# Kernel optimization log

Measured on AMD Instinct MI355X. Metric: run time of the kernel, lower is better.

## Reference

```python
import jax, jax.numpy as jnp
import numpy as np

D_ENC = 512
D_DEC = 512
D_JOINT = D_ENC + D_DEC  # 1024
V = 1024


def setup_inputs() -> dict:
    key = jax.random.key(0)
    ks = jax.random.split(key, 8)
    s = lambda fan_in: 1.0 / np.sqrt(fan_in)
    return {
        "encoder_output": jax.random.normal(ks[0], (8, 200, D_ENC), dtype=jnp.float32),
        "decoder_output": jax.random.normal(ks[1], (8, 50, D_DEC), dtype=jnp.float32),
        "W_enc": jax.random.uniform(ks[2], (D_JOINT, D_ENC), jnp.float32, -s(D_ENC), s(D_ENC)),
        "b_enc": jax.random.uniform(ks[3], (D_JOINT,), jnp.float32, -s(D_ENC), s(D_ENC)),
        "W_dec": jax.random.uniform(ks[4], (D_JOINT, D_DEC), jnp.float32, -s(D_DEC), s(D_DEC)),
        "b_dec": jax.random.uniform(ks[5], (D_JOINT,), jnp.float32, -s(D_DEC), s(D_DEC)),
        "W_fc": jax.random.uniform(ks[6], (V, D_JOINT), jnp.float32, -s(D_JOINT), s(D_JOINT)),
        "b_fc": jax.random.uniform(ks[7], (V,), jnp.float32, -s(D_JOINT), s(D_JOINT)),
    }


def reference(encoder_output, decoder_output, W_enc, b_enc, W_dec, b_dec, W_fc, b_fc):
    # enc: (B, T, D_JOINT); dec: (B, U, D_JOINT)
    enc = jnp.einsum('btd,jd->btj', encoder_output, W_enc) + b_enc
    dec = jnp.einsum('bud,jd->buj', decoder_output, W_dec) + b_dec
    # broadcast join: (B, T, U, D_JOINT)
    combined = enc[:, :, None, :] + dec[:, None, :, :]
    logits = jnp.einsum('btuj,vj->btuv', jnp.tanh(combined), W_fc) + b_fc
    return jax.nn.log_softmax(logits, axis=-1)
```

## Files before the change

### kernel.cpp

```cpp
#include <hip/hip_runtime.h>
#include <hip/hip_bf16.h>
#include <hip/hip_fp8.h>

#define TT 200
#define UU 50
#define BB 8
#define DJ 1024
#define DE 512
#define VV 1024
#define M_TOTAL (BB*TT*UU)
#define MB 80
#define NITER 32
#define WINV (1.0f/32.0f)

typedef float f32x4 __attribute__((ext_vector_type(4)));

__device__ __forceinline__ float fast_tanh(float x) {
    float e = __expf(2.f * x);
    return 1.f - 2.f / (e + 1.f);
}

__device__ __forceinline__ unsigned char f2fp8(float x) {
    return __hip_fp8_e4m3(x).__x;
}

__device__ __forceinline__ unsigned long long tanh_pack_fp8(float4 e0, float4 e1, float4 d0, float4 d1) {
    unsigned long long r;
    r  = (unsigned long long)f2fp8(fast_tanh(e0.x + d0.x));
    r |= (unsigned long long)f2fp8(fast_tanh(e0.y + d0.y)) << 8;
    r |= (unsigned long long)f2fp8(fast_tanh(e0.z + d0.z)) << 16;
    r |= (unsigned long long)f2fp8(fast_tanh(e0.w + d0.w)) << 24;
    r |= (unsigned long long)f2fp8(fast_tanh(e1.x + d1.x)) << 32;
    r |= (unsigned long long)f2fp8(fast_tanh(e1.y + d1.y)) << 40;
    r |= (unsigned long long)f2fp8(fast_tanh(e1.z + d1.z)) << 48;
    r |= (unsigned long long)f2fp8(fast_tanh(e1.w + d1.w)) << 56;
    return r;
}

__global__ void k_wfct(const float* __restrict__ w, unsigned char* __restrict__ o) {
    const int G = blockIdx.x * 256 + threadIdx.x;
    const int gk = G >> 10, n = G & 1023;
    const float* src = w + (size_t)n * DJ + gk * 8;
    float4 a = *(const float4*)(src);
    float4 b = *(const float4*)(src + 4);
    unsigned long long r;
    r  = (unsigned long long)f2fp8(a.x * 32.f);
    r |= (unsigned long long)f2fp8(a.y * 32.f) << 8;
    r |= (unsigned long long)f2fp8(a.z * 32.f) << 16;
    r |= (unsigned long long)f2fp8(a.w * 32.f) << 24;
    r |= (unsigned long long)f2fp8(b.x * 32.f) << 32;
    r |= (unsigned long long)f2fp8(b.y * 32.f) << 40;
    r |= (unsigned long long)f2fp8(b.z * 32.f) << 48;
    r |= (unsigned long long)f2fp8(b.w * 32.f) << 56;
    *(unsigned long long*)(o + (size_t)G * 8) = r;
}

__global__ __launch_bounds__(256) void k_proj2(const float* __restrict__ enc,
                                               const float* __restrict__ dec,
                                               const float* __restrict__ W_enc,
                                               const float* __restrict__ b_enc,
                                               const float* __restrict__ W_dec,
                                               const float* __restrict__ b_dec,
                                               float* __restrict__ encp,
                                               float* __restrict__ decp) {
    __shared__ float in_s[16][DE];
    const bool isDec = blockIdx.x >= 100;
    const float* in  = isDec ? dec   : enc;
    const float* W   = isDec ? W_dec : W_enc;
    const float* bia = isDec ? b_dec : b_enc;
    float* out       = isDec ? decp  : encp;
    const int NR     = isDec ? (BB*UU) : (BB*TT);
    const int m0 = (isDec ? (blockIdx.x - 100) : blockIdx.x) * 16;
    const int tid = threadIdx.x;
    #pragma unroll
    for (int it = 0; it < 8; ++it) {
        int idx = tid + it * 256;
        int r = idx >> 7, c = (idx & 127) << 2;
        *(float4*)&in_s[r][c] = *(const float4*)(in + (size_t)(m0 + r) * DE + c);
    }
    __syncthreads();
    const int j = blockIdx.y * 256 + tid;
    const float4* wr = (const float4*)(W + (size_t)j * DE);
    float acc[16];
    #pragma unroll
    for (int r = 0; r < 16; ++r) acc[r] = 0.f;
    for (int d4 = 0; d4 < DE / 4; ++d4) {
        float4 w = wr[d4];
        #pragma unroll
        for (int r = 0; r < 16; ++r) {
            float4 x = *(const float4*)&in_s[r][d4 << 2];
            acc[r] += x.x * w.x + x.y * w.y + x.z * w.z + x.w * w.w;
        }
    }
    float bv = bia[j];
    const int gk = j >> 3, kl = j & 7;
    #pragma unroll
    for (int r = 0; r < 16; ++r)
        out[((size_t)gk * NR + (m0 + r)) * 8 + kl] = acc[r] + bv;
}

__global__ __launch_bounds__(512, 2) void k_joint(const float* __restrict__ encp,
                                                  const float* __restrict__ decp,
                                                  const unsigned char* __restrict__ wfc8,
                                                  const float* __restrict__ bfc,
                                                  float* __restrict__ out) {
    __shared__ unsigned char As[81920];
    __shared__ float red[8][MB];

    const int tid = threadIdx.x;
    const int wave = tid >> 6, lane = tid & 63;
    const int g = lane >> 4, ln = lane & 15;
    const int bid = blockIdx.x;
    const int m0 = bid * MB;

    for (int r = 0; r < 20; ++r) {
        const int gidx = r * 512 + tid;
        const int gkf = gidx / MB;
        const int m = gidx - gkf * MB;
        const int mrow = m0 + m;
        const int b = mrow / (TT * UU);
        const int rem = mrow - b * (TT * UU);
        const int t = rem / UU;
        const int u = rem - t * UU;
        const float* ep = encp + ((size_t)gkf * (BB * TT) + b * TT + t) * 8;
        const float* dp = decp + ((size_t)gkf * (BB * UU) + b * UU + u) * 8;
        float4 e0 = *(const float4*)(ep);
        float4 e1 = *(const float4*)(ep + 4);
        float4 d0 = *(const float4*)(dp);
        float4 d1 = *(const float4*)(dp + 4);
        *(unsigned long long*)&As[(size_t)gidx * 8] = tanh_pack_fp8(e0, e1, d0, d1);
    }

    f32x4 acc[5][8];
    #pragma unroll
    for (int mf = 0; mf < 5; ++mf)
        #pragma unroll
        for (int nf = 0; nf < 8; ++nf)
            acc[mf][nf] = (f32x4){0.f, 0.f, 0.f, 0.f};

    __syncthreads();

    const unsigned char* bbase = wfc8 + (size_t)(wave * 128 + ln) * 8;

    for (int t = 0; t < NITER; ++t) {
        const int kb = (t + bid) & 31;
        long afr[5];
        #pragma unroll
        for (int mf = 0; mf < 5; ++mf)
            afr[mf] = *(const long*)&As[(size_t)((kb * 4 + g) * MB + mf * 16 + ln) * 8];
        const unsigned char* bchunk = bbase + (size_t)(kb * 4 + g) * 1024 * 8;
        #pragma unroll
        for (int nf = 0; nf < 8; ++nf) {
            long bfr = *(const long*)(bchunk + (size_t)nf * 16 * 8);
            #pragma unroll
            for (int mf = 0; mf < 5; ++mf)
                acc[mf][nf] = __builtin_amdgcn_mfma_f32_16x16x32_fp8_fp8(afr[mf], bfr, acc[mf][nf], 0, 0, 0);
        }
    }

    float bv[8];
    #pragma unroll
    for (int nf = 0; nf < 8; ++nf) bv[nf] = bfc[wave * 128 + nf * 16 + ln];
    #pragma unroll
    for (int mf = 0; mf < 5; ++mf)
        #pragma unroll
        for (int nf = 0; nf < 8; ++nf)
            #pragma unroll
            for (int j = 0; j < 4; ++j)
                acc[mf][nf][j] = acc[mf][nf][j] * WINV + bv[nf];

    float rmx[5][4];
    #pragma unroll
    for (int mf = 0; mf < 5; ++mf)
        #pragma unroll
        for (int j = 0; j < 4; ++j) {
            float mx = -3.0e38f;
            #pragma unroll
            for (int nf = 0; nf < 8; ++nf) mx = fmaxf(mx, acc[mf][nf][j]);
            #pragma unroll
            for (int s = 1; s < 16; s <<= 1) mx = fmaxf(mx, __shfl_xor(mx, s));
            rmx[mf][j] = mx;
        }
    if (ln == 0) {
        #pragma unroll
        for (int mf = 0; mf < 5; ++mf)
            #pragma unroll
            for (int j = 0; j < 4; ++j)
                red[wave][mf * 16 + g * 4 + j] = rmx[mf][j];
    }
    __syncthreads();
    #pragma unroll
    for (int mf = 0; mf < 5; ++mf)
        #pragma unroll
        for (int j = 0; j < 4; ++j) {
            const int r = mf * 16 + g * 4 + j;
            float mx = red[0][r];
            #pragma unroll
            for (int w = 1; w < 8; ++w) mx = fmaxf(mx, red[w][r]);
            rmx[mf][j] = mx;
        }
    __syncthreads();

    float rsm[5][4];
    #pragma unroll
    for (int mf = 0; mf < 5; ++mf)
        #pragma unroll
        for (int j = 0; j < 4; ++j) {
            float s = 0.f;
            #pragma unroll
            for (int nf = 0; nf < 8; ++nf) s += __expf(acc[mf][nf][j] - rmx[mf][j]);
            #pragma unroll
            for (int t2 = 1; t2 < 16; t2 <<= 1) s += __shfl_xor(s, t2);
            rsm[mf][j] = s;
        }
    if (ln == 0) {
        #pragma unroll
        for (int mf = 0; mf < 5; ++mf)
            #pragma unroll
            for (int j = 0; j < 4; ++j)
                red[wave][mf * 16 + g * 4 + j] = rsm[mf][j];
    }
    __syncthreads();
    #pragma unroll
    for (int mf = 0; mf < 5; ++mf)
        #pragma unroll
        for (int j = 0; j < 4; ++j) {
            const int r = mf * 16 + g * 4 + j;
            float s = 0.f;
            #pragma unroll
            for (int w = 0; w < 8; ++w) s += red[w][r];
            const float lse = rmx[mf][j] + __logf(s);
            float* op = out + (size_t)(m0 + r) * VV + wave * 128 + ln;
            #pragma unroll
            for (int nf = 0; nf < 8; ++nf)
                __builtin_nontemporal_store(acc[mf][nf][j] - lse, op + nf * 16);
        }
}

extern "C" void kernel_launch(void* const* d_in, const int* in_sizes, int n_in,
                              void* d_out, int out_size, void* d_ws, size_t ws_size,
                              hipStream_t stream) {
    const float* enc   = (const float*)d_in[0];
    const float* dec   = (const float*)d_in[1];
    const float* W_enc = (const float*)d_in[2];
    const float* b_enc = (const float*)d_in[3];
    const float* W_dec = (const float*)d_in[4];
    const float* b_dec = (const float*)d_in[5];
    const float* W_fc  = (const float*)d_in[6];
    const float* b_fc  = (const float*)d_in[7];
    float* out = (float*)d_out;

    float* encp = (float*)d_ws;
    float* decp = encp + (size_t)BB * TT * DJ;
    unsigned char* wfc8 = (unsigned char*)(decp + (size_t)BB * UU * DJ);

    k_wfct<<<(VV * DJ) / (256 * 8), 256, 0, stream>>>(W_fc, wfc8);
    k_proj2<<<dim3(125, DJ / 256), 256, 0, stream>>>(enc, dec, W_enc, b_enc, W_dec, b_dec, encp, decp);
    k_joint<<<M_TOTAL / MB, 512, 0, stream>>>(encp, decp, wfc8, b_fc, out);
}
```

Before: 325.7 us.

## Relayout FP8 operands for 16-byte loads and double-buffer K-loop fragments

Rearranges the FP8 W_fc buffer and the shared-memory A tile so each lane reads two consecutive K-steps as one 16-byte vector. This halves the number of load instructions per MFMA. The K loop now runs 16 iterations, each with two MFMA substeps, and software-pipelines them by prefetching the next iteration's A and B fragments into alternate register sets while the current MFMAs execute. This is meant to hide global and LDS load latency behind compute. The cost is higher register pressure at 512 threads with 2 blocks per SM, which could cause spills.

Result: slower. 405.9 us (+24.6%).

```diff
diff --git a/kernel.cpp b/kernel.cpp
--- a/kernel.cpp
+++ b/kernel.cpp
@@ -10,10 +10,10 @@
 #define VV 1024
 #define M_TOTAL (BB*TT*UU)
 #define MB 80
-#define NITER 32
 #define WINV (1.0f/32.0f)
 
 typedef float f32x4 __attribute__((ext_vector_type(4)));
+typedef long long2_t __attribute__((ext_vector_type(2)));
 
 __device__ __forceinline__ float fast_tanh(float x) {
     float e = __expf(2.f * x);
@@ -52,7 +52,8 @@
     r |= (unsigned long long)f2fp8(b.y * 32.f) << 40;
     r |= (unsigned long long)f2fp8(b.z * 32.f) << 48;
     r |= (unsigned long long)f2fp8(b.w * 32.f) << 56;
-    *(unsigned long long*)(o + (size_t)G * 8) = r;
+    const int kb2 = gk >> 3, sub = (gk >> 2) & 1, g = gk & 3;
+    *(unsigned long long*)(o + (size_t)kb2 * 65536 + (size_t)n * 64 + g * 16 + sub * 8) = r;
 }
 
 __global__ __launch_bounds__(256) void k_proj2(const float* __restrict__ enc,
@@ -104,7 +105,7 @@
                                                   const unsigned char* __restrict__ wfc8,
                                                   const float* __restrict__ bfc,
                                                   float* __restrict__ out) {
-    __shared__ unsigned char As[81920];
+    __shared__ long2_t As4[5120];
     __shared__ float red[8][MB];
 
     const int tid = threadIdx.x;
@@ -128,7 +129,8 @@
         float4 e1 = *(const float4*)(ep + 4);
         float4 d0 = *(const float4*)(dp);
         float4 d1 = *(const float4*)(dp + 4);
-        *(unsigned long long*)&As[(size_t)gidx * 8] = tanh_pack_fp8(e0, e1, d0, d1);
+        const int akb2 = gkf >> 3, asub = (gkf >> 2) & 1, ag = gkf & 3;
+        ((unsigned long long*)&As4[(akb2 * 4 + ag) * 80 + m])[asub] = tanh_pack_fp8(e0, e1, d0, d1);
     }
 
     f32x4 acc[5][8];
@@ -140,23 +142,46 @@
 
     __syncthreads();
 
-    const unsigned char* bbase = wfc8 + (size_t)(wave * 128 + ln) * 8;
-
-    for (int t = 0; t < NITER; ++t) {
-        const int kb = (t + bid) & 31;
-        long afr[5];
+    const unsigned char* bptr = wfc8 + wave * 8192 + ln * 64 + g * 16;
+    const long2_t* aptr = As4 + g * 80 + ln;
+
+    long2_t bA[8], bB[8], aA[5], aB[5];
+    {
+        const int k0 = bid & 15;
+        #pragma unroll
+        for (int nf = 0; nf < 8; ++nf)
+            bA[nf] = *(const long2_t*)(bptr + (size_t)k0 * 65536 + nf * 1024);
         #pragma unroll
         for (int mf = 0; mf < 5; ++mf)
-            afr[mf] = *(const long*)&As[(size_t)((kb * 4 + g) * MB + mf * 16 + ln) * 8];
-        const unsigned char* bchunk = bbase + (size_t)(kb * 4 + g) * 1024 * 8;
-        #pragma unroll
-        for (int nf = 0; nf < 8; ++nf) {
-            long bfr = *(const long*)(bchunk + (size_t)nf * 16 * 8);
-            #pragma unroll
-            for (int mf = 0; mf < 5; ++mf)
-                acc[mf][nf] = __builtin_amdgcn_mfma_f32_16x16x32_fp8_fp8(afr[mf], bfr, acc[mf][nf], 0, 0, 0);
-        }
-    }
+            aA[mf] = aptr[k0 * 320 + mf * 16];
+    }
+
+#define STEP(CA, CB, NA, NB, T2)                                                          \
+    do {                                                                                  \
+        if ((T2) < 15) {                                                                  \
+            const int kn = ((T2) + 1 + bid) & 15;                                         \
+            _Pragma("unroll")                                                             \
+            for (int nf = 0; nf < 8; ++nf)                                                \
+                NB[nf] = *(const long2_t*)(bptr + (size_t)kn * 65536 + nf * 1024);        \
+            _Pragma("unroll")                                                             \
+            for (int mf = 0; mf < 5; ++mf)                                                \
+                NA[mf] = aptr[kn * 320 + mf * 16];                                        \
+        }                                                                                 \
+        _Pragma("unroll")                                                                 \
+        for (int nf = 0; nf < 8; ++nf)                                                    \
+            _Pragma("unroll")                                                             \
+            for (int s = 0; s < 2; ++s)                                                   \
+                _Pragma("unroll")                                                         \
+                for (int mf = 0; mf < 5; ++mf)                                            \
+                    acc[mf][nf] = __builtin_amdgcn_mfma_f32_16x16x32_fp8_fp8(             \
+                        CA[mf][s], CB[nf][s], acc[mf][nf], 0, 0, 0);                      \
+    } while (0)
+
+    for (int t2 = 0; t2 < 16; t2 += 2) {
+        STEP(aA, bA, aB, bB, t2);
+        STEP(aB, bB, aA, bA, t2 + 1);
+    }
+#undef STEP
 
     float bv[8];
     #pragma unroll
```
